# Performance work log

Measured on AMD Instinct MI355X. Metric: run time of the kernel, lower is better.

## Reference

```python
import jax, jax.numpy as jnp
import numpy as np


def setup_inputs() -> dict:
    key = jax.random.key(0)
    ks = jax.random.split(key, 8)
    C = 512
    Cq = C // 8  # 64
    x = jax.random.normal(ks[0], (4, C, 64, 64), dtype=jnp.float32)
    # 1x1 conv == per-pixel linear; store weights as [out, in]
    Wq = jax.random.normal(ks[1], (Cq, C), dtype=jnp.float32) * (1.0 / np.sqrt(C))
    bq = jax.random.normal(ks[2], (Cq,), dtype=jnp.float32) * 0.01
    Wk = jax.random.normal(ks[3], (Cq, C), dtype=jnp.float32) * (1.0 / np.sqrt(C))
    bk = jax.random.normal(ks[4], (Cq,), dtype=jnp.float32) * 0.01
    Wv = jax.random.normal(ks[5], (C, C), dtype=jnp.float32) * (1.0 / np.sqrt(C))
    bv = jax.random.normal(ks[6], (C,), dtype=jnp.float32) * 0.01
    alpha = jax.random.normal(ks[7], (1,), dtype=jnp.float32)
    return {"x": x, "Wq": Wq, "bq": bq, "Wk": Wk, "bk": bk, "Wv": Wv, "bv": bv, "alpha": alpha}


def reference(x, Wq, bq, Wk, bk, Wv, bv, alpha):
    B, C, H, W = x.shape
    HW = H * W
    xf = x.reshape(B, C, HW)  # [B, C, HW]
    # 1x1 convs as channel matmuls
    q = jnp.einsum('oc,bcn->bon', Wq, xf) + bq[None, :, None]  # [B, Cq, HW]
    k = jnp.einsum('oc,bcn->bon', Wk, xf) + bk[None, :, None]  # [B, Cq, HW]
    v = jnp.einsum('oc,bcn->bon', Wv, xf) + bv[None, :, None]  # [B, C, HW]
    # attention[b, i, j] = softmax_j( q[:, i] . k[:, j] )
    scores = jnp.einsum('bci,bcj->bij', q, k)  # [B, HW, HW]
    attn = jax.nn.softmax(scores, axis=-1)
    # feat_e = v @ attn^T : out[b, c, i] = sum_j v[b, c, j] * attn[b, i, j]
    feat_e = jnp.einsum('bcj,bij->bci', v, attn).reshape(B, C, H, W)
    return alpha[0] * feat_e
```

## Files before the change

kernel.cpp:

```cpp
#include <hip/hip_runtime.h>
#include <hip/hip_fp16.h>

#define HW_N 4096
#define C_IN 512
#define C_Q  64
#define NB   4
#define M_Y  640
#define M_YP 768
#define LOG2E 1.4426950408889634f

typedef __attribute__((ext_vector_type(8))) short short8;
typedef __attribute__((ext_vector_type(4))) short short4v;
typedef __attribute__((ext_vector_type(4))) float float4v;
typedef unsigned short ushort_t;

__device__ __forceinline__ ushort_t f2h(float x) {
    return __half_as_ushort(__float2half(x));
}
__device__ __forceinline__ float h2f(ushort_t h) {
    return __half2float(__ushort_as_half(h));
}
__device__ __forceinline__ void gl2lds16(const ushort_t* g, ushort_t* l) {
    __builtin_amdgcn_global_load_lds(
        (const __attribute__((address_space(1))) unsigned int*)g,
        (__attribute__((address_space(3))) unsigned int*)l, 16, 0, 0);
}

__global__ __launch_bounds__(256) void split_w(const float* __restrict__ Wq,
                                               const float* __restrict__ Wk,
                                               const float* __restrict__ Wv,
                                               ushort_t* __restrict__ Wh,
                                               ushort_t* __restrict__ Wl) {
    int idx = (blockIdx.x * 256 + threadIdx.x) * 4;
#pragma unroll
    for (int e = 0; e < 4; e++) {
        int i = idx + e;
        int m = i >> 9, k = i & 511;
        float v = (m < C_Q) ? Wq[m * C_IN + k]
                 : (m < 2 * C_Q) ? Wk[(m - C_Q) * C_IN + k]
                 : (m < M_Y) ? Wv[(size_t)(m - 2 * C_Q) * C_IN + k]
                 : 0.f;
        ushort_t h = f2h(v);
        Wh[i] = h;
        Wl[i] = f2h(v - h2f(h));
    }
}

__global__ __launch_bounds__(256) void split_x(const float* __restrict__ x,
                                               ushort_t* __restrict__ xTh,
                                               ushort_t* __restrict__ xTl,
                                               float* __restrict__ D) {
    const size_t bz = blockIdx.z;
    x   += bz * ((size_t)C_IN * HW_N);
    xTh += bz * ((size_t)HW_N * C_IN);
    xTl += bz * ((size_t)HW_N * C_IN);
    D   += bz * HW_N;

    if (blockIdx.y == 0 && blockIdx.x < 16) D[blockIdx.x * 256 + threadIdx.x] = 0.f;

    __shared__ float tile[64][65];
    const int n0 = blockIdx.x * 64, k0 = blockIdx.y * 64;
    const int t = threadIdx.x;
#pragma unroll
    for (int it = 0; it < 4; it++) {
        int e = t + it * 256;
        int r = e >> 4, c4 = (e & 15) << 2;
        float4 v = *(const float4*)(x + (size_t)(k0 + r) * HW_N + n0 + c4);
        tile[r][c4 + 0] = v.x; tile[r][c4 + 1] = v.y;
        tile[r][c4 + 2] = v.z; tile[r][c4 + 3] = v.w;
    }
    __syncthreads();
    const int rr = t >> 2, kq = (t & 3) << 4;
    ushort_t h[16], l[16];
#pragma unroll
    for (int j = 0; j < 16; j++) {
        float v = tile[kq + j][rr];
        h[j] = f2h(v);
        l[j] = f2h(v - h2f(h[j]));
    }
    size_t o = (size_t)(n0 + rr) * C_IN + k0 + kq;
    *(uint4*)(xTh + o) = *(uint4*)h;
    *(uint4*)(xTh + o + 8) = *(uint4*)(h + 8);
    *(uint4*)(xTl + o) = *(uint4*)l;
    *(uint4*)(xTl + o + 8) = *(uint4*)(l + 8);
}

__global__ __launch_bounds__(512, 2) void ygemm(
    const ushort_t* __restrict__ Ah, const ushort_t* __restrict__ Al,
    const ushort_t* __restrict__ Bh, const ushort_t* __restrict__ Bl,
    const float* __restrict__ bq, const float* __restrict__ bk,
    const float* __restrict__ bv,
    ushort_t* __restrict__ qkTh, ushort_t* __restrict__ qkTl,
    ushort_t* __restrict__ Vh, ushort_t* __restrict__ Vl) {
    const size_t bz = blockIdx.z;
    Bh   += bz * ((size_t)HW_N * C_IN);
    Bl   += bz * ((size_t)HW_N * C_IN);
    qkTh += bz * ((size_t)HW_N * 2 * C_Q);
    qkTl += bz * ((size_t)HW_N * 2 * C_Q);
    Vh   += bz * ((size_t)C_IN * HW_N);
    Vl   += bz * ((size_t)C_IN * HW_N);

    __shared__ ushort_t sAh[2][256 * 32];
    __shared__ ushort_t sAl[2][256 * 32];
    __shared__ ushort_t sBh[2][256 * 32];
    __shared__ ushort_t sBl[2][256 * 32];

    const int tid = threadIdx.x, w = tid >> 6, lane = tid & 63;
    const int quad = lane >> 4, lr = lane & 15;
    const int m0 = blockIdx.y * 256, n0 = blockIdx.x * 256;

    const int mat = w >> 1, half = w & 1;
    const ushort_t* src;
    ushort_t* dst0;
    int rowBase;
    if (mat == 0)      { src = Ah; dst0 = sAh[0]; rowBase = m0; }
    else if (mat == 1) { src = Al; dst0 = sAl[0]; rowBase = m0; }
    else if (mat == 2) { src = Bh; dst0 = sBh[0]; rowBase = n0; }
    else               { src = Bl; dst0 = sBl[0]; rowBase = n0; }
    const int cr = lane >> 2, uv = lane & 3;
    const int kcol = (uv ^ ((cr >> 1) & 3)) << 3;
    const ushort_t* gk = src + (size_t)(rowBase + half * 128 + cr) * C_IN + kcol;
    const int cOfs = half * 8;

    const int wm = (w & 3) * 64, wn = (w >> 2) * 128;
    const int up = (quad ^ ((lr >> 1) & 3)) << 3;

    float4v acc[4][8];
#pragma unroll
    for (int i = 0; i < 4; i++)
#pragma unroll
        for (int j = 0; j < 8; j++) acc[i][j] = (float4v){0.f, 0.f, 0.f, 0.f};

#pragma unroll
    for (int c = 0; c < 8; c++)
        gl2lds16(gk + (size_t)(c * 16) * C_IN, dst0 + (cOfs + c) * 512);
    __syncthreads();

    const int NSTEP = C_IN / 32;
    for (int it = 0; it < NSTEP; ++it) {
        const int cur = it & 1, nxt = cur ^ 1;

        if (it + 1 < NSTEP) {
            ushort_t* db = dst0 + nxt * (256 * 32);
#pragma unroll
            for (int c = 0; c < 8; c++)
                gl2lds16(gk + (size_t)(c * 16) * C_IN + (it + 1) * 32,
                         db + (cOfs + c) * 512);
        }

        short8 bh[8], bl[8];
#pragma unroll
        for (int j = 0; j < 8; j++) {
            const int row = wn + j * 16 + lr;
            bh[j] = *(const short8*)&sBh[cur][row * 32 + up];
            bl[j] = *(const short8*)&sBl[cur][row * 32 + up];
        }
#pragma unroll
        for (int i = 0; i < 4; i++) {
            const int row = wm + i * 16 + lr;
            short8 ah = *(const short8*)&sAh[cur][row * 32 + up];
            short8 al = *(const short8*)&sAl[cur][row * 32 + up];
#pragma unroll
            for (int j = 0; j < 8; j++)
                acc[i][j] = __builtin_amdgcn_mfma_f32_16x16x32_f16(ah, bh[j], acc[i][j], 0, 0, 0);
#pragma unroll
            for (int j = 0; j < 8; j++)
                acc[i][j] = __builtin_amdgcn_mfma_f32_16x16x32_f16(ah, bl[j], acc[i][j], 0, 0, 0);
#pragma unroll
            for (int j = 0; j < 8; j++)
                acc[i][j] = __builtin_amdgcn_mfma_f32_16x16x32_f16(al, bh[j], acc[i][j], 0, 0, 0);
        }
        __syncthreads();
    }

#pragma unroll
    for (int i = 0; i < 4; i++)
#pragma unroll
        for (int j = 0; j < 8; j++)
#pragma unroll
            for (int r = 0; r < 4; r++) {
                const int m = m0 + wm + i * 16 + quad * 4 + r;
                if (m >= M_Y) continue;
                const int n = n0 + wn + j * 16 + lr;
                float bi = (m < C_Q) ? bq[m]
                          : (m < 2 * C_Q) ? bk[m - C_Q] : bv[m - 2 * C_Q];
                float v = acc[i][j][r] + bi;
                ushort_t h = f2h(v);
                ushort_t lo = f2h(v - h2f(h));
                if (m < 2 * C_Q) {
                    qkTh[(size_t)n * (2 * C_Q) + m] = h;
                    qkTl[(size_t)n * (2 * C_Q) + m] = lo;
                } else {
                    Vh[(size_t)(m - 2 * C_Q) * HW_N + n] = h;
                    Vl[(size_t)(m - 2 * C_Q) * HW_N + n] = lo;
                }
            }
}

__global__ __launch_bounds__(256, 2) void qkgemm(const ushort_t* __restrict__ qkTh_,
                                                 const ushort_t* __restrict__ qkTl_,
                                                 float* __restrict__ outF,
                                                 float* __restrict__ Dsum) {
    __shared__ ushort_t sAh[2][128 * 32];
    __shared__ ushort_t sAl[2][128 * 32];
    __shared__ ushort_t sBh[2][128 * 32];
    __shared__ ushort_t sBl[2][128 * 32];

    const int tid = threadIdx.x, w = tid >> 6, lane = tid & 63;
    const int quad = lane >> 4, lr = lane & 15;
    const int m0 = blockIdx.y * 128, n0 = blockIdx.x * 128;

    const ushort_t* src = ((w & 1) ? qkTl_ : qkTh_) + ((w >> 1) ? C_Q : 0);
    ushort_t* dst0 = (w == 0) ? sAh[0] : (w == 1) ? sAl[0]
                   : (w == 2) ? sBh[0] : sBl[0];
    const int rowBase = (w >> 1) ? n0 : m0;
    const int cr = lane >> 2, uv = lane & 3;
    const int kcol = (uv ^ ((cr >> 1) & 3)) << 3;
    const ushort_t* gk = src + (size_t)(rowBase + cr) * (2 * C_Q) + kcol;

    const int wm = (w & 1) * 64, wn = (w >> 1) * 64;
    const int up = (quad ^ ((lr >> 1) & 3)) << 3;

    float4v acc[4][4];
#pragma unroll
    for (int i = 0; i < 4; i++)
#pragma unroll
        for (int j = 0; j < 4; j++) acc[i][j] = (float4v){0.f, 0.f, 0.f, 0.f};

#pragma unroll
    for (int c = 0; c < 8; c++)
        gl2lds16(gk + (size_t)(c * 16) * (2 * C_Q), dst0 + c * 512);
    __syncthreads();

    const int NSTEP = C_Q / 32;
#pragma unroll
    for (int it = 0; it < NSTEP; ++it) {
        const int cur = it & 1, nxt = cur ^ 1;

        if (it + 1 < NSTEP) {
            ushort_t* db = dst0 + nxt * (128 * 32);
#pragma unroll
            for (int c = 0; c < 8; c++)
                gl2lds16(gk + (size_t)(c * 16) * (2 * C_Q) + (it + 1) * 32, db + c * 512);
        }

        short8 ah[4], al[4], bh[4], bl[4];
#pragma unroll
        for (int i = 0; i < 4; i++) {
            ah[i] = *(const short8*)&sAh[cur][(wm + i * 16 + lr) * 32 + up];
            al[i] = *(const short8*)&sAl[cur][(wm + i * 16 + lr) * 32 + up];
            bh[i] = *(const short8*)&sBh[cur][(wn + i * 16 + lr) * 32 + up];
            bl[i] = *(const short8*)&sBl[cur][(wn + i * 16 + lr) * 32 + up];
        }
#pragma unroll
        for (int i = 0; i < 4; i++)
#pragma unroll
            for (int j = 0; j < 4; j++)
                acc[i][j] = __builtin_amdgcn_mfma_f32_16x16x32_f16(ah[i], bh[j], acc[i][j], 0, 0, 0);
#pragma unroll
        for (int i = 0; i < 4; i++)
#pragma unroll
            for (int j = 0; j < 4; j++)
                acc[i][j] = __builtin_amdgcn_mfma_f32_16x16x32_f16(ah[i], bl[j], acc[i][j], 0, 0, 0);
#pragma unroll
        for (int i = 0; i < 4; i++)
#pragma unroll
            for (int j = 0; j < 4; j++)
                acc[i][j] = __builtin_amdgcn_mfma_f32_16x16x32_f16(al[i], bh[j], acc[i][j], 0, 0, 0);
        if (it + 1 < NSTEP) __syncthreads();
    }

#pragma unroll
    for (int i = 0; i < 4; i++) {
#pragma unroll
        for (int r = 0; r < 4; r++) {
            float s = 0.f;
#pragma unroll
            for (int j = 0; j < 4; j++) {
                const int m = m0 + wm + i * 16 + quad * 4 + r;
                const int n = n0 + wn + j * 16 + lr;
                outF[(size_t)m * HW_N + n] = acc[i][j][r];
                s += __expf(acc[i][j][r]);
            }
            s += __shfl_xor(s, 1);
            s += __shfl_xor(s, 2);
            s += __shfl_xor(s, 4);
            s += __shfl_xor(s, 8);
            if (lr == 0)
                atomicAdd(&Dsum[m0 + wm + i * 16 + quad * 4 + r], s);
        }
    }
}

__global__ __launch_bounds__(512, 2) void feat7(const ushort_t* __restrict__ Vh,
                                                const ushort_t* __restrict__ Vl,
                                                const float* __restrict__ S,
                                                const float* __restrict__ D,
                                                float* __restrict__ out,
                                                float* __restrict__ part,
                                                int kLen) {
    __shared__ ushort_t sVh[2][256 * 32];
    __shared__ ushort_t sVl[2][256 * 32];
    __shared__ ushort_t sP [2][256 * 32];

    const int tid = threadIdx.x, w = tid >> 6, lane = tid & 63;
    const int quad = lane >> 4, lr = lane & 15;
    const int m0 = blockIdx.y * 256, n0 = blockIdx.x * 256;
    const int k0 = blockIdx.z * kLen;

    const int crv = lane >> 2, uv = lane & 3;
    const int vcol = (uv ^ ((crv >> 1) & 3)) << 3;
    const ushort_t* vbase = (w < 4) ? Vh : Vl;
    const ushort_t* gVsrc[4];
    int sOfs[4];
#pragma unroll
    for (int c = 0; c < 4; c++) {
        const int chunk = ((w & 3) * 4 + c);
        gVsrc[c] = vbase + (size_t)(m0 + chunk * 16 + crv) * HW_N + vcol + k0;
        sOfs[c] = chunk * 512;
    }

    const int pr = tid >> 3, pu = tid & 7;
    const float* gS = S + (size_t)(n0 + pr) * HW_N + k0 + pu * 4;
    const int pdst = (((pu >> 1) ^ ((pr >> 1) & 3)) << 3) + ((pu & 1) << 2);
    float lrw[4];
#pragma unroll
    for (int c = 0; c < 4; c++) lrw[c] = -log2f(D[n0 + pr + 64 * c]);

    const int wm = (w & 3) * 64, wn = (w >> 2) * 128;

    float4 sreg[4];
    const int nIter = kLen >> 5;

    {
#pragma unroll
        for (int c = 0; c < 4; c++)
            sreg[c] = *(const float4*)(gS + (size_t)(64 * c) * HW_N);
#pragma unroll
        for (int c = 0; c < 4; c++) gl2lds16(gVsrc[c], ((w < 4) ? sVh : sVl)[0] + sOfs[c]);
#pragma unroll
        for (int c = 0; c < 4; c++) {
            ushort_t h4[4];
            h4[0] = f2h(exp2f(fmaf(sreg[c].x, LOG2E, lrw[c])));
            h4[1] = f2h(exp2f(fmaf(sreg[c].y, LOG2E, lrw[c])));
            h4[2] = f2h(exp2f(fmaf(sreg[c].z, LOG2E, lrw[c])));
            h4[3] = f2h(exp2f(fmaf(sreg[c].w, LOG2E, lrw[c])));
            *(short4v*)&sP[0][(pr + 64 * c) * 32 + pdst] = *(short4v*)h4;
        }
        if (nIter > 1) {
#pragma unroll
            for (int c = 0; c < 4; c++)
                sreg[c] = *(const float4*)(gS + (size_t)(64 * c) * HW_N + 32);
        }
    }
    __syncthreads();

    float4v acc[4][8];
#pragma unroll
    for (int i = 0; i < 4; i++)
#pragma unroll
        for (int j = 0; j < 8; j++) acc[i][j] = (float4v){0.f, 0.f, 0.f, 0.f};

    for (int it = 0; it < nIter; ++it) {
        const int kk = it << 5;
        const int cur = it & 1, nxt = cur ^ 1;

        if (it + 1 < nIter) {
            ushort_t* db = ((w < 4) ? sVh : sVl)[nxt];
#pragma unroll
            for (int c = 0; c < 4; c++) gl2lds16(gVsrc[c] + kk + 32, db + sOfs[c]);
        }

        short8 bh[8];
#pragma unroll
        for (int j = 0; j < 8; j++) {
            const int row = wn + j * 16 + lr;
            bh[j] = *(const short8*)&sP[cur][row * 32 + ((quad ^ ((lr >> 1) & 3)) << 3)];
        }

        if (it + 1 < nIter) {
#pragma unroll
            for (int c = 0; c < 4; c++) {
                ushort_t h4[4];
                h4[0] = f2h(exp2f(fmaf(sreg[c].x, LOG2E, lrw[c])));
                h4[1] = f2h(exp2f(fmaf(sreg[c].y, LOG2E, lrw[c])));
                h4[2] = f2h(exp2f(fmaf(sreg[c].z, LOG2E, lrw[c])));
                h4[3] = f2h(exp2f(fmaf(sreg[c].w, LOG2E, lrw[c])));
                *(short4v*)&sP[nxt][(pr + 64 * c) * 32 + pdst] = *(short4v*)h4;
            }
            if (it + 2 < nIter) {
#pragma unroll
                for (int c = 0; c < 4; c++)
                    sreg[c] = *(const float4*)(gS + (size_t)(64 * c) * HW_N + kk + 64);
            }
        }

#pragma unroll
        for (int i = 0; i < 4; i++) {
            const int row = wm + i * 16 + lr;
            const int up = (quad ^ ((lr >> 1) & 3)) << 3;
            short8 ah = *(const short8*)&sVh[cur][row * 32 + up];
            short8 al = *(const short8*)&sVl[cur][row * 32 + up];
#pragma unroll
            for (int j = 0; j < 8; j++)
                acc[i][j] = __builtin_amdgcn_mfma_f32_16x16x32_f16(ah, bh[j], acc[i][j], 0, 0, 0);
#pragma unroll
            for (int j = 0; j < 8; j++)
                acc[i][j] = __builtin_amdgcn_mfma_f32_16x16x32_f16(al, bh[j], acc[i][j], 0, 0, 0);
        }
        __syncthreads();
    }

    float* o = (blockIdx.z == 0) ? out
             : (part + (size_t)(blockIdx.z - 1) * ((size_t)C_IN * HW_N));
#pragma unroll
    for (int i = 0; i < 4; i++)
#pragma unroll
        for (int j = 0; j < 8; j++)
#pragma unroll
            for (int r = 0; r < 4; r++) {
                const int m = m0 + wm + i * 16 + quad * 4 + r;
                const int n = n0 + wn + j * 16 + lr;
                o[(size_t)m * HW_N + n] = acc[i][j][r];
            }
}

__global__ __launch_bounds__(256) void reduce_alphaN(float* __restrict__ out,
                                                     const float4* __restrict__ part,
                                                     size_t stride4,
                                                     const float* __restrict__ alpha,
                                                     int np) {
    const size_t i = (size_t)blockIdx.x * 256 + threadIdx.x;
    const float a = alpha[0];
    float4* out4 = (float4*)out;
    float4 s = out4[i];
    for (int p = 0; p < np; p++) {
        float4 t = part[i + (size_t)p * stride4];
        s.x += t.x; s.y += t.y; s.z += t.z; s.w += t.w;
    }
    float4 o;
    o.x = a * s.x; o.y = a * s.y; o.z = a * s.z; o.w = a * s.w;
    out4[i] = o;
}


extern "C" void kernel_launch(void* const* d_in, const int* in_sizes, int n_in,
                              void* d_out, int out_size, void* d_ws, size_t ws_size,
                              hipStream_t stream) {
    const float* x     = (const float*)d_in[0];
    const float* Wq    = (const float*)d_in[1];
    const float* bq    = (const float*)d_in[2];
    const float* Wk    = (const float*)d_in[3];
    const float* bk    = (const float*)d_in[4];
    const float* Wv    = (const float*)d_in[5];
    const float* bv    = (const float*)d_in[6];
    const float* alpha = (const float*)d_in[7];
    float* out = (float*)d_out;

    const size_t planeQK = (size_t)HW_N * 2 * C_Q;
    const size_t planeV  = (size_t)C_IN * HW_N;
    const size_t planeXT = (size_t)HW_N * C_IN;
    const size_t planeW  = (size_t)M_YP * C_IN;
    const size_t planeS  = (size_t)HW_N * HW_N;

    const size_t fusedBytes =
        (size_t)NB * HW_N * 4 + 2 * (size_t)NB * planeQK * 2 +
        2 * (size_t)NB * planeV * 2 + 2 * planeW * 2 + planeS * 4 +
        7 * planeV * 4;
    const bool fused = (ws_size >= fusedBytes);

    if (fused) {
        float* D4      = (float*)d_ws;
        ushort_t* qkTh4 = (ushort_t*)(D4 + (size_t)NB * HW_N);
        ushort_t* qkTl4 = qkTh4 + (size_t)NB * planeQK;
        ushort_t* Vh4   = qkTl4 + (size_t)NB * planeQK;
        ushort_t* Vl4   = Vh4 + (size_t)NB * planeV;
        ushort_t* Wh    = Vl4 + (size_t)NB * planeV;
        ushort_t* Wl    = Wh + planeW;
        float* scores   = (float*)(Wl + planeW);
        float* part     = scores + planeS;
        ushort_t* xTh4  = (ushort_t*)scores;
        ushort_t* xTl4  = xTh4 + (size_t)NB * planeXT;

        split_w<<<dim3(M_YP * C_IN / 4 / 256), dim3(256), 0, stream>>>(Wq, Wk, Wv, Wh, Wl);

        split_x<<<dim3(HW_N / 64, C_IN / 64, NB), dim3(256), 0, stream>>>(
            x, xTh4, xTl4, D4);
        ygemm<<<dim3(HW_N / 256, M_YP / 256, NB), dim3(512), 0, stream>>>(
            Wh, Wl, xTh4, xTl4, bq, bk, bv, qkTh4, qkTl4, Vh4, Vl4);

        for (int b = 0; b < NB; b++) {
            float* outb = out + (size_t)b * planeV;
            qkgemm<<<dim3(HW_N / 128, HW_N / 128), dim3(256), 0, stream>>>(
                qkTh4 + (size_t)b * planeQK, qkTl4 + (size_t)b * planeQK,
                scores, D4 + (size_t)b * HW_N);
            feat7<<<dim3(HW_N / 256, C_IN / 256, 8), dim3(512), 0, stream>>>(
                Vh4 + (size_t)b * planeV, Vl4 + (size_t)b * planeV,
                scores, D4 + (size_t)b * HW_N, outb, part, HW_N / 8);
            reduce_alphaN<<<dim3((C_IN * HW_N / 4) / 256), dim3(256), 0, stream>>>(
                outb, (const float4*)part, planeV / 4, alpha, 7);
        }
        return;
    }

    float* D = (float*)d_ws;
    ushort_t* qkTh = (ushort_t*)(D + HW_N);
    ushort_t* qkTl = qkTh + planeQK;
    ushort_t* Vh   = qkTl + planeQK;
    ushort_t* Vl   = Vh + planeV;
    ushort_t* Wh   = Vl + planeV;
    ushort_t* Wl   = Wh + planeW;
    float* scores  = (float*)(Wl + planeW);
    float* part    = scores + planeS;
    ushort_t* xTh  = (ushort_t*)scores;
    ushort_t* xTl  = xTh + planeXT;

    const size_t baseF = (size_t)(part - (float*)d_ws);
    const int zsplit = (ws_size >= (baseF + 7 * planeV) * sizeof(float)) ? 8 : 4;

    split_w<<<dim3(M_YP * C_IN / 4 / 256), dim3(256), 0, stream>>>(Wq, Wk, Wv, Wh, Wl);

    for (int b = 0; b < NB; b++) {
        const float* xb = x + (size_t)b * planeV;
        float* outb = out + (size_t)b * planeV;

        split_x<<<dim3(HW_N / 64, C_IN / 64, 1), dim3(256), 0, stream>>>(
            xb, xTh, xTl, D);
        ygemm<<<dim3(HW_N / 256, M_YP / 256, 1), dim3(512), 0, stream>>>(
            Wh, Wl, xTh, xTl, bq, bk, bv, qkTh, qkTl, Vh, Vl);
        qkgemm<<<dim3(HW_N / 128, HW_N / 128), dim3(256), 0, stream>>>(
            qkTh, qkTl, scores, D);
        feat7<<<dim3(HW_N / 256, C_IN / 256, zsplit), dim3(512), 0, stream>>>(
            Vh, Vl, scores, D, outb, part, HW_N / zsplit);
        reduce_alphaN<<<dim3((C_IN * HW_N / 4) / 256), dim3(256), 0, stream>>>(
            outb, (const float4*)part, planeV / 4, alpha, zsplit - 1);
    }
}
```

Measured before the change: 485.9 us.

## Enlarge qkgemm tile to 256x256 with 512 threads and single-shot K load

The score GEMM kernel moves from a 128x128 tile with 4 waves to a 256x256 tile with 8 waves. Each wave now computes a 64x128 sub-tile. The whole K=64 dimension is loaded into LDS in one go, split across waves, which replaces the double-buffered two-step loop and its mid-loop barrier. This raises operand reuse per LDS load and cuts the number of blocks. The costs are 64KB of LDS, twice the accumulator registers, and only 256 blocks per batch, so fewer blocks can be resident at once.

```diff
diff --git a/kernel.cpp b/kernel.cpp
--- a/kernel.cpp
+++ b/kernel.cpp
@@ -197,77 +197,67 @@
             }
 }
 
-__global__ __launch_bounds__(256, 2) void qkgemm(const ushort_t* __restrict__ qkTh_,
+__global__ __launch_bounds__(512, 2) void qkgemm(const ushort_t* __restrict__ qkTh_,
                                                  const ushort_t* __restrict__ qkTl_,
                                                  float* __restrict__ outF,
                                                  float* __restrict__ Dsum) {
-    __shared__ ushort_t sAh[2][128 * 32];
-    __shared__ ushort_t sAl[2][128 * 32];
-    __shared__ ushort_t sBh[2][128 * 32];
-    __shared__ ushort_t sBl[2][128 * 32];
+    __shared__ ushort_t sAh[2][256 * 32];
+    __shared__ ushort_t sAl[2][256 * 32];
+    __shared__ ushort_t sBh[2][256 * 32];
+    __shared__ ushort_t sBl[2][256 * 32];
 
     const int tid = threadIdx.x, w = tid >> 6, lane = tid & 63;
     const int quad = lane >> 4, lr = lane & 15;
-    const int m0 = blockIdx.y * 128, n0 = blockIdx.x * 128;
-
-    const ushort_t* src = ((w & 1) ? qkTl_ : qkTh_) + ((w >> 1) ? C_Q : 0);
-    ushort_t* dst0 = (w == 0) ? sAh[0] : (w == 1) ? sAl[0]
-                   : (w == 2) ? sBh[0] : sBl[0];
-    const int rowBase = (w >> 1) ? n0 : m0;
+    const int m0 = blockIdx.y * 256, n0 = blockIdx.x * 256;
+
+    const int mat = w >> 1, ks = w & 1;
+    const ushort_t* src = ((mat & 1) ? qkTl_ : qkTh_) + ((mat >> 1) ? C_Q : 0);
+    ushort_t* dst0 = ((mat == 0) ? sAh : (mat == 1) ? sAl
+                    : (mat == 2) ? sBh : sBl)[ks];
+    const int rowBase = (mat >> 1) ? n0 : m0;
     const int cr = lane >> 2, uv = lane & 3;
     const int kcol = (uv ^ ((cr >> 1) & 3)) << 3;
-    const ushort_t* gk = src + (size_t)(rowBase + cr) * (2 * C_Q) + kcol;
-
-    const int wm = (w & 1) * 64, wn = (w >> 1) * 64;
+    const ushort_t* gk = src + (size_t)(rowBase + cr) * (2 * C_Q) + ks * 32 + kcol;
+
+    const int wm = (w & 3) * 64, wn = (w >> 2) * 128;
     const int up = (quad ^ ((lr >> 1) & 3)) << 3;
 
-    float4v acc[4][4];
+#pragma unroll
+    for (int c = 0; c < 16; c++)
+        gl2lds16(gk + (size_t)(c * 16) * (2 * C_Q), dst0 + c * 512);
+
+    float4v acc[4][8];
 #pragma unroll
     for (int i = 0; i < 4; i++)
 #pragma unroll
-        for (int j = 0; j < 4; j++) acc[i][j] = (float4v){0.f, 0.f, 0.f, 0.f};
-
-#pragma unroll
-    for (int c = 0; c < 8; c++)
-        gl2lds16(gk + (size_t)(c * 16) * (2 * C_Q), dst0 + c * 512);
+        for (int j = 0; j < 8; j++) acc[i][j] = (float4v){0.f, 0.f, 0.f, 0.f};
+
     __syncthreads();
 
-    const int NSTEP = C_Q / 32;
-#pragma unroll
-    for (int it = 0; it < NSTEP; ++it) {
-        const int cur = it & 1, nxt = cur ^ 1;
-
-        if (it + 1 < NSTEP) {
-            ushort_t* db = dst0 + nxt * (128 * 32);
-#pragma unroll
-            for (int c = 0; c < 8; c++)
-                gl2lds16(gk + (size_t)(c * 16) * (2 * C_Q) + (it + 1) * 32, db + c * 512);
-        }
-
-        short8 ah[4], al[4], bh[4], bl[4];
+#pragma unroll
+    for (int k2 = 0; k2 < 2; k2++) {
+        short8 bh[8], bl[8];
+#pragma unroll
+        for (int j = 0; j < 8; j++) {
+            const int row = wn + j * 16 + lr;
+            bh[j] = *(const short8*)&sBh[k2][row * 32 + up];
+            bl[j] = *(const short8*)&sBl[k2][row * 32 + up];
+        }
 #pragma unroll
         for (int i = 0; i < 4; i++) {
-            ah[i] = *(const short8*)&sAh[cur][(wm + i * 16 + lr) * 32 + up];
-            al[i] = *(const short8*)&sAl[cur][(wm + i * 16 + lr) * 32 + up];
-            bh[i] = *(const short8*)&sBh[cur][(wn + i * 16 + lr) * 32 + up];
-            bl[i] = *(const short8*)&sBl[cur][(wn + i * 16 + lr) * 32 + up];
-        }
-#pragma unroll
-        for (int i = 0; i < 4; i++)
-#pragma unroll
-            for (int j = 0; j < 4; j++)
-                acc[i][j] = __builtin_amdgcn_mfma_f32_16x16x32_f16(ah[i], bh[j], acc[i][j], 0, 0, 0);
-#pragma unroll
-        for (int i = 0; i < 4; i++)
-#pragma unroll
-            for (int j = 0; j < 4; j++)
-                acc[i][j] = __builtin_amdgcn_mfma_f32_16x16x32_f16(ah[i], bl[j], acc[i][j], 0, 0, 0);
-#pragma unroll
-        for (int i = 0; i < 4; i++)
-#pragma unroll
-            for (int j = 0; j < 4; j++)
-                acc[i][j] = __builtin_amdgcn_mfma_f32_16x16x32_f16(al[i], bh[j], acc[i][j], 0, 0, 0);
-        if (it + 1 < NSTEP) __syncthreads();
+            const int row = wm + i * 16 + lr;
+            short8 ah = *(const short8*)&sAh[k2][row * 32 + up];
+            short8 al = *(const short8*)&sAl[k2][row * 32 + up];
+#pragma unroll
+            for (int j = 0; j < 8; j++)
+                acc[i][j] = __builtin_amdgcn_mfma_f32_16x16x32_f16(ah, bh[j], acc[i][j], 0, 0, 0);
+#pragma unroll
+            for (int j = 0; j < 8; j++)
+                acc[i][j] = __builtin_amdgcn_mfma_f32_16x16x32_f16(ah, bl[j], acc[i][j], 0, 0, 0);
+#pragma unroll
+            for (int j = 0; j < 8; j++)
+                acc[i][j] = __builtin_amdgcn_mfma_f32_16x16x32_f16(al, bh[j], acc[i][j], 0, 0, 0);
+        }
     }
 
 #pragma unroll
@@ -276,7 +266,7 @@
         for (int r = 0; r < 4; r++) {
             float s = 0.f;
 #pragma unroll
-            for (int j = 0; j < 4; j++) {
+            for (int j = 0; j < 8; j++) {
                 const int m = m0 + wm + i * 16 + quad * 4 + r;
                 const int n = n0 + wn + j * 16 + lr;
                 outF[(size_t)m * HW_N + n] = acc[i][j][r];
@@ -491,7 +481,7 @@
 
         for (int b = 0; b < NB; b++) {
             float* outb = out + (size_t)b * planeV;
-            qkgemm<<<dim3(HW_N / 128, HW_N / 128), dim3(256), 0, stream>>>(
+            qkgemm<<<dim3(HW_N / 256, HW_N / 256), dim3(512), 0, stream>>>(
                 qkTh4 + (size_t)b * planeQK, qkTl4 + (size_t)b * planeQK,
                 scores, D4 + (size_t)b * HW_N);
             feat7<<<dim3(HW_N / 256, C_IN / 256, 8), dim3(512), 0, stream>>>(
@@ -528,7 +518,7 @@
             xb, xTh, xTl, D);
         ygemm<<<dim3(HW_N / 256, M_YP / 256, 1), dim3(512), 0, stream>>>(
             Wh, Wl, xTh, xTl, bq, bk, bv, qkTh, qkTl, Vh, Vl);
-        qkgemm<<<dim3(HW_N / 128, HW_N / 128), dim3(256), 0, stream>>>(
+        qkgemm<<<dim3(HW_N / 256, HW_N / 256), dim3(512), 0, stream>>>(
             qkTh, qkTl, scores, D);
         feat7<<<dim3(HW_N / 256, C_IN / 256, zsplit), dim3(512), 0, stream>>>(
             Vh, Vl, scores, D, outb, part, HW_N / zsplit);
```

Result: faster. 471.5 us (-3.0%).
